# Performance work log

Hardware: AMD Instinct MI355X
Metric: run time of the kernel (lower is better)

Reference implementation:

```python
import jax, jax.numpy as jnp
import numpy as np

N = 100_000      # num nodes
E = 100_000      # num hyperedges
NNZ = 1_600_000  # incidence entries (avg degree 16)
DIN = 128
DOUT = 128


def setup_inputs() -> dict:
    key = jax.random.key(0)
    k1, k2, k3, k4 = jax.random.split(key, 4)
    x = jax.random.normal(k1, (N, DIN), dtype=jnp.float32)
    weight = jax.random.normal(k2, (DIN, DOUT), dtype=jnp.float32) / np.sqrt(DIN).astype(np.float32)
    bias = jax.random.normal(k3, (DOUT,), dtype=jnp.float32) * 0.02
    hyperedge_index = jax.random.randint(k4, (2, NNZ), 0, N, dtype=jnp.int64)
    return {"x": x, "weight": weight, "bias": bias, "hyperedge_index": hyperedge_index}


def reference(x, weight, bias, hyperedge_index):
    # PyG HypergraphConv (use_attention=False, heads=1):
    #   out = D^{-1} H W B^{-1} H^T (x @ Theta) + bias, W = I (unit hyperedge weights)
    node_idx = hyperedge_index[0]  # [NNZ]
    edge_idx = hyperedge_index[1]  # [NNZ]

    h = x @ weight  # [N, DOUT]

    ones = jnp.ones((NNZ,), dtype=h.dtype)
    # node degree D_i = sum of hyperedge weights (=1) over incident hyperedges
    D = jax.ops.segment_sum(ones, node_idx, num_segments=N)   # [N]
    # hyperedge degree B_e = number of incident nodes
    B = jax.ops.segment_sum(ones, edge_idx, num_segments=E)   # [E]
    Dinv = jnp.where(D > 0, 1.0 / D, 0.0)
    Binv = jnp.where(B > 0, 1.0 / B, 0.0)

    # nodes -> hyperedges: m_e = B_e^{-1} * sum_{i in e} h_i
    e_feat = jax.ops.segment_sum(h[node_idx], edge_idx, num_segments=E) * Binv[:, None]  # [E, DOUT]
    # hyperedges -> nodes: out_i = D_i^{-1} * sum_{e ni i} m_e
    out = jax.ops.segment_sum(e_feat[edge_idx], node_idx, num_segments=N) * Dinv[:, None]  # [N, DOUT]
    return out + bias
```

## Files before the change

kernel.cpp:

```cpp
#include <hip/hip_runtime.h>

#define Nn 100000
#define Ne 100000
#define NNZC 1600000
#define NBLK 256
#define CHUNK 6250
#define BSH 8
#define BUCKW 256
#define NBK 391
#define CAPB 5120
#define GEMM_TOTAL 1563
#define GEMM_A 782
#define GEMM_B 781
#define FCAP 4608
#define SEGW 4
#define NG0 6250

typedef __attribute__((ext_vector_type(8))) short short8;
typedef __attribute__((ext_vector_type(4))) float floatx4;

__device__ inline unsigned short f2bf(float f) {
    union { float f; unsigned int i; } c; c.f = f;
    unsigned int i = c.i;
    return (unsigned short)((i + 0x7fffu + ((i >> 16) & 1u)) >> 16);
}
__device__ inline unsigned int f2bf2(float lo, float hi) {
    union { float f; unsigned int i; } a, b;
    a.f = lo; b.f = hi;
    const unsigned int x = (a.i + 0x7fffu + ((a.i >> 16) & 1u)) >> 16;
    const unsigned int y = (b.i + 0x7fffu + ((b.i >> 16) & 1u)) & 0xffff0000u;
    return x | y;
}

union FusedLds {
    unsigned short wlds[128 * 136];
    struct { int a[NBK]; int b[NBK]; } s;
};
struct FineLds {
    int cnt[BUCKW];
    int tmp[2][BUCKW];
    unsigned int cache[FCAP];
};
union FineGemmLds {
    unsigned short wlds[128 * 136];
    FineLds f;
};

__device__ inline void gemm_block(int gb, const float* __restrict__ x,
                                  const float* __restrict__ w,
                                  unsigned short* __restrict__ h,
                                  unsigned short* wlds, int tid) {
    const int wave = tid >> 6, lane = tid & 63;
    const int q = lane >> 4, r16 = lane & 15;

    for (int i = tid; i < 4096; i += 256) {
        const int k = i >> 5;
        const int n0 = (i & 31) << 2;
        const float4 wv = *(const float4*)(w + k * 128 + n0);
        wlds[(n0 + 0) * 136 + k] = f2bf(wv.x);
        wlds[(n0 + 1) * 136 + k] = f2bf(wv.y);
        wlds[(n0 + 2) * 136 + k] = f2bf(wv.z);
        wlds[(n0 + 3) * 136 + k] = f2bf(wv.w);
    }
    __syncthreads();

    const int row0 = gb * 64 + wave * 16;
    const int rrow = min(row0 + r16, Nn - 1);

    floatx4 acc[8];
#pragma unroll
    for (int jb = 0; jb < 8; ++jb) acc[jb] = (floatx4){0.f, 0.f, 0.f, 0.f};

    const float* ap = x + (size_t)rrow * 128 + q * 8;
#pragma unroll
    for (int kk = 0; kk < 4; ++kk) {
        const float4 a0 = *(const float4*)(ap + kk * 32);
        const float4 a1 = *(const float4*)(ap + kk * 32 + 4);
        union { unsigned int u[4]; short8 s; } xf;
        xf.u[0] = f2bf2(a0.x, a0.y);
        xf.u[1] = f2bf2(a0.z, a0.w);
        xf.u[2] = f2bf2(a1.x, a1.y);
        xf.u[3] = f2bf2(a1.z, a1.w);
        const unsigned short* wp = wlds + kk * 32 + q * 8;
#pragma unroll
        for (int jb = 0; jb < 8; ++jb) {
            const short8 wf = *(const short8*)(wp + (jb * 16 + r16) * 136);
            acc[jb] = __builtin_amdgcn_mfma_f32_16x16x32_bf16(wf, xf.s, acc[jb], 0, 0, 0);
        }
    }

    if (row0 + r16 < Nn) {
        unsigned short* hb = h + (size_t)(row0 + r16) * 128 + q * 4;
#pragma unroll
        for (int jb = 0; jb < 8; ++jb) {
            uint2 o;
            o.x = f2bf2(acc[jb][0], acc[jb][1]);
            o.y = f2bf2(acc[jb][2], acc[jb][3]);
            *(uint2*)(hb + jb * 16) = o;
        }
    }
}

__global__ __launch_bounds__(256) void scatter_gemm_kernel(
        const int* __restrict__ nidx, const int* __restrict__ eidx,
        int* __restrict__ gcurN, int* __restrict__ gcurE,
        unsigned int* __restrict__ pairsN, unsigned int* __restrict__ pairsE,
        const float* __restrict__ x, const float* __restrict__ w,
        unsigned short* __restrict__ h) {
    __shared__ FusedLds sm;
    const int tid = threadIdx.x;
    if (blockIdx.x < NBLK) {
        for (int j = tid; j < NBK; j += 256) { sm.s.a[j] = 0; sm.s.b[j] = 0; }
        __syncthreads();
        const int base = blockIdx.x * CHUNK;
        for (int i = base + tid; i < base + CHUNK; i += 256) {
            atomicAdd(&sm.s.a[nidx[i] >> BSH], 1);
            atomicAdd(&sm.s.b[eidx[i] >> BSH], 1);
        }
        __syncthreads();
        for (int j = tid; j < NBK; j += 256) {
            sm.s.a[j] = atomicAdd(&gcurN[j], sm.s.a[j]);
            sm.s.b[j] = atomicAdd(&gcurE[j], sm.s.b[j]);
        }
        __syncthreads();
        for (int i = base + tid; i < base + CHUNK; i += 256) {
            const int n = nidx[i], e = eidx[i];
            const int pn = atomicAdd(&sm.s.a[n >> BSH], 1);
            if (pn < CAPB)
                pairsN[(size_t)(n >> BSH) * CAPB + pn] =
                    ((unsigned int)e << 8) | (unsigned int)(n & 255);
            const int pe = atomicAdd(&sm.s.b[e >> BSH], 1);
            if (pe < CAPB)
                pairsE[(size_t)(e >> BSH) * CAPB + pe] =
                    ((unsigned int)n << 8) | (unsigned int)(e & 255);
        }
    } else {
        gemm_block(blockIdx.x - NBLK, x, w, h, sm.wlds, tid);
    }
}

__device__ inline void fine_block(int b, const unsigned int* __restrict__ pairs,
                                  const int* __restrict__ gcur,
                                  int* __restrict__ offs, int* __restrict__ perm,
                                  FineLds& L, int t) {
    const int cnt_b = min(gcur[b], CAPB);
    int part = 0;
    for (int j = t; j < b; j += 256) part += min(gcur[j], CAPB);
    L.tmp[0][t] = part;
    __syncthreads();
    for (int off = 128; off > 0; off >>= 1) {
        if (t < off) L.tmp[0][t] += L.tmp[0][t + off];
        __syncthreads();
    }
    const int S = L.tmp[0][0];
    __syncthreads();

    const unsigned int* pb = pairs + (size_t)b * CAPB;
    L.cnt[t] = 0;
    __syncthreads();
    for (int i = t; i < cnt_b; i += BUCKW) {
        const unsigned int p = pb[i];
        if (i < FCAP) L.cache[i] = p;
        atomicAdd(&L.cnt[p & 255u], 1);
    }
    __syncthreads();
    int v = L.cnt[t];
    int pin = 0;
    L.tmp[0][t] = v;
    for (int off = 1; off < BUCKW; off <<= 1) {
        __syncthreads();
        int val = L.tmp[pin][t];
        if (t >= off) val += L.tmp[pin][t - off];
        L.tmp[1 - pin][t] = val;
        pin ^= 1;
    }
    __syncthreads();
    const int excl = L.tmp[pin][t] - v;
    const int id = b * BUCKW + t;
    if (id < 100000) offs[id] = S + excl;
    if (b == NBK - 1 && t == 0) offs[100000] = NNZC;
    __syncthreads();
    L.cnt[t] = excl;
    __syncthreads();
    for (int i = t; i < cnt_b; i += BUCKW) {
        const unsigned int p = (i < FCAP) ? L.cache[i] : pb[i];
        const int pos = S + atomicAdd(&L.cnt[p & 255u], 1);
        perm[pos] = (int)(p >> 8);
    }
}

template <int MODE>
__device__ inline void gather_body(int gblk, const int* __restrict__ perm,
                                   const int* __restrict__ offs,
                                   const void* __restrict__ srcv,
                                   const float* __restrict__ bias,
                                   void* __restrict__ outv, int tid) {
    const int wave = tid >> 6;
    const int lane = tid & 63;
    const int e0 = __builtin_amdgcn_readfirstlane((gblk * 4 + wave) * SEGW);
    const int start = offs[e0];
    const int end = offs[e0 + SEGW];
    const unsigned int laneoff = (unsigned int)lane << 2;
    const char* src = (const char*)srcv;

    float bx = 0.f, by = 0.f;
    if (MODE == 1) {
        const float2 b = ((const float2*)bias)[lane];
        bx = b.x; by = b.y;
    }

    float ax = 0.f, ay = 0.f;
    int e = e0;
    int seg_start = start;
    int nb = offs[e0 + 1];

    auto flush = [&](int deg) {
        const float sinv = deg ? 1.f / (float)deg : 0.f;
        if (MODE == 0) {
            *(unsigned int*)((char*)outv + (((unsigned int)e << 8) | laneoff)) =
                f2bf2(ax * sinv, ay * sinv);
        } else {
            float2 o;
            o.x = ax * sinv + bx;
            o.y = ay * sinv + by;
            *(float2*)((char*)outv + (((unsigned int)e << 9) | (laneoff << 1))) = o;
        }
        ax = 0.f; ay = 0.f;
        ++e;
    };

    int myv = 0;
    for (int i = start; i < end; i += 8) {
        const int t = (i - start) & 63;
        if (t == 0) myv = perm[min(i + lane, NNZC - 1)];
        const int m = min(end - i, 8);
        unsigned int a[8], u[8];
#pragma unroll
        for (int j = 0; j < 8; ++j)
            a[j] = ((unsigned int)__shfl(myv, t + (j < m ? j : m - 1), 64) << 8) | laneoff;
#pragma unroll
        for (int j = 0; j < 8; ++j) u[j] = *(const unsigned int*)(src + a[j]);
#pragma unroll
        for (int j = 0; j < 8; ++j) {
            if (j < m) {
                while (i + j == nb) {
                    flush(nb - seg_start);
                    seg_start = nb;
                    nb = offs[e + 1];
                }
                ax += __uint_as_float(u[j] << 16);
                ay += __uint_as_float(u[j] & 0xffff0000u);
            }
        }
    }
    while (e < e0 + SEGW) {
        flush(end - seg_start);
        seg_start = end;
    }
}

__global__ __launch_bounds__(256) void fineE_gemm_kernel(
        const unsigned int* __restrict__ pairsE, const int* __restrict__ gcurE,
        int* __restrict__ offsE, int* __restrict__ permE,
        const float* __restrict__ x, const float* __restrict__ w,
        unsigned short* __restrict__ h) {
    __shared__ FineGemmLds sm;
    const int tid = threadIdx.x;
    if (blockIdx.x < NBK) {
        fine_block(blockIdx.x, pairsE, gcurE, offsE, permE, sm.f, tid);
    } else {
        gemm_block(GEMM_A + blockIdx.x - NBK, x, w, h, sm.wlds, tid);
    }
}

__global__ __launch_bounds__(256) void g0_fineN_kernel(
        const int* __restrict__ permE, const int* __restrict__ offsE,
        const unsigned short* __restrict__ h, unsigned short* __restrict__ ef,
        const unsigned int* __restrict__ pairsN, const int* __restrict__ gcurN,
        int* __restrict__ offsN, int* __restrict__ permN) {
    __shared__ FineLds sm;
    const int tid = threadIdx.x;
    if (blockIdx.x < NBK) {
        fine_block(blockIdx.x, pairsN, gcurN, offsN, permN, sm, tid);
    } else {
        gather_body<0>(blockIdx.x - NBK, permE, offsE, h, nullptr, ef, tid);
    }
}

__global__ __launch_bounds__(256) void gather_e2n_kernel(
        const int* __restrict__ permN, const int* __restrict__ offsN,
        const unsigned short* __restrict__ ef, const float* __restrict__ bias,
        float* __restrict__ out) {
    gather_body<1>(blockIdx.x, permN, offsN, ef, bias, out, threadIdx.x);
}

extern "C" void kernel_launch(void* const* d_in, const int* in_sizes, int n_in,
                              void* d_out, int out_size, void* d_ws, size_t ws_size,
                              hipStream_t stream) {
    const float* x = (const float*)d_in[0];
    const float* w = (const float*)d_in[1];
    const float* bias = (const float*)d_in[2];
    const int* hei = (const int*)d_in[3];
    const int* nidx = hei;
    const int* eidx = hei + NNZC;
    float* out = (float*)d_out;

    char* p = (char*)d_ws;
    unsigned short* h = (unsigned short*)p;  p += (size_t)Nn * 128 * 2;
    unsigned short* ef = (unsigned short*)p; p += (size_t)Ne * 128 * 2;
    int* gcurN = (int*)p;                    p += NBK * 4 + 192;
    int* gcurE = (int*)p;                    p += NBK * 4 + 192;
    int* offsN = (int*)p;                    p += 400128;
    int* offsE = (int*)p;                    p += 400128;
    int* permN = (int*)p;                    p += (size_t)NNZC * 4;
    int* permE = (int*)p;                    p += (size_t)NNZC * 4;
    unsigned int* pairsN = (unsigned int*)p; p += (size_t)NBK * CAPB * 4;
    unsigned int* pairsE = (unsigned int*)p; p += (size_t)NBK * CAPB * 4;

    hipMemsetAsync(gcurN, 0, 2 * (NBK * 4 + 192), stream);

    scatter_gemm_kernel<<<NBLK + GEMM_A, 256, 0, stream>>>(nidx, eidx, gcurN, gcurE,
                                                           pairsN, pairsE, x, w, h);
    fineE_gemm_kernel<<<NBK + GEMM_B, 256, 0, stream>>>(pairsE, gcurE, offsE, permE,
                                                        x, w, h);
    g0_fineN_kernel<<<NBK + NG0, 256, 0, stream>>>(permE, offsE, h, ef,
                                                   pairsN, gcurN, offsN, permN);
    gather_e2n_kernel<<<NG0, 256, 0, stream>>>(permN, offsN, ef, bias, out);
}
```

Before: 297.7 us.

## Move GEMM out of scatter kernel and use 256-row GEMM blocks

Takes the GEMM blocks out of the scatter kernel, which now launches only the 256 scatter blocks. The whole GEMM moves into the second kernel alongside the E-side fine-sort blocks. Each GEMM block now covers 256 rows in four 64-row passes, so the weight-to-LDS bf16 conversion runs 391 times instead of 1563. This cuts redundant weight staging and changes which work overlaps, but the scatter kernel may leave the GPU underused and the GEMM now sits in a single kernel.

```diff
diff --git a/kernel.cpp b/kernel.cpp
--- a/kernel.cpp
+++ b/kernel.cpp
@@ -9,9 +9,7 @@
 #define BUCKW 256
 #define NBK 391
 #define CAPB 5120
-#define GEMM_TOTAL 1563
-#define GEMM_A 782
-#define GEMM_B 781
+#define GEMM_TOTAL 391
 #define FCAP 4608
 #define SEGW 4
 #define NG0 6250
@@ -32,10 +30,6 @@
     return x | y;
 }
 
-union FusedLds {
-    unsigned short wlds[128 * 136];
-    struct { int a[NBK]; int b[NBK]; } s;
-};
 struct FineLds {
     int cnt[BUCKW];
     int tmp[2][BUCKW];
@@ -46,10 +40,10 @@
     FineLds f;
 };
 
-__device__ inline void gemm_block(int gb, const float* __restrict__ x,
-                                  const float* __restrict__ w,
-                                  unsigned short* __restrict__ h,
-                                  unsigned short* wlds, int tid) {
+__device__ inline void gemm_block256(int gb, const float* __restrict__ x,
+                                     const float* __restrict__ w,
+                                     unsigned short* __restrict__ h,
+                                     unsigned short* wlds, int tid) {
     const int wave = tid >> 6, lane = tid & 63;
     const int q = lane >> 4, r16 = lane & 15;
 
@@ -64,78 +58,75 @@
     }
     __syncthreads();
 
-    const int row0 = gb * 64 + wave * 16;
-    const int rrow = min(row0 + r16, Nn - 1);
-
-    floatx4 acc[8];
-#pragma unroll
-    for (int jb = 0; jb < 8; ++jb) acc[jb] = (floatx4){0.f, 0.f, 0.f, 0.f};
-
-    const float* ap = x + (size_t)rrow * 128 + q * 8;
-#pragma unroll
-    for (int kk = 0; kk < 4; ++kk) {
-        const float4 a0 = *(const float4*)(ap + kk * 32);
-        const float4 a1 = *(const float4*)(ap + kk * 32 + 4);
-        union { unsigned int u[4]; short8 s; } xf;
-        xf.u[0] = f2bf2(a0.x, a0.y);
-        xf.u[1] = f2bf2(a0.z, a0.w);
-        xf.u[2] = f2bf2(a1.x, a1.y);
-        xf.u[3] = f2bf2(a1.z, a1.w);
-        const unsigned short* wp = wlds + kk * 32 + q * 8;
-#pragma unroll
-        for (int jb = 0; jb < 8; ++jb) {
-            const short8 wf = *(const short8*)(wp + (jb * 16 + r16) * 136);
-            acc[jb] = __builtin_amdgcn_mfma_f32_16x16x32_bf16(wf, xf.s, acc[jb], 0, 0, 0);
+#pragma unroll 1
+    for (int rg = 0; rg < 4; ++rg) {
+        const int row0 = gb * 256 + rg * 64 + wave * 16;
+        const int rrow = min(row0 + r16, Nn - 1);
+
+        floatx4 acc[8];
+#pragma unroll
+        for (int jb = 0; jb < 8; ++jb) acc[jb] = (floatx4){0.f, 0.f, 0.f, 0.f};
+
+        const float* ap = x + (size_t)rrow * 128 + q * 8;
+#pragma unroll
+        for (int kk = 0; kk < 4; ++kk) {
+            const float4 a0 = *(const float4*)(ap + kk * 32);
+            const float4 a1 = *(const float4*)(ap + kk * 32 + 4);
+            union { unsigned int u[4]; short8 s; } xf;
+            xf.u[0] = f2bf2(a0.x, a0.y);
+            xf.u[1] = f2bf2(a0.z, a0.w);
+            xf.u[2] = f2bf2(a1.x, a1.y);
+            xf.u[3] = f2bf2(a1.z, a1.w);
+            const unsigned short* wp = wlds + kk * 32 + q * 8;
+#pragma unroll
+            for (int jb = 0; jb < 8; ++jb) {
+                const short8 wf = *(const short8*)(wp + (jb * 16 + r16) * 136);
+                acc[jb] = __builtin_amdgcn_mfma_f32_16x16x32_bf16(wf, xf.s, acc[jb], 0, 0, 0);
+            }
         }
-    }
-
-    if (row0 + r16 < Nn) {
-        unsigned short* hb = h + (size_t)(row0 + r16) * 128 + q * 4;
-#pragma unroll
-        for (int jb = 0; jb < 8; ++jb) {
-            uint2 o;
-            o.x = f2bf2(acc[jb][0], acc[jb][1]);
-            o.y = f2bf2(acc[jb][2], acc[jb][3]);
-            *(uint2*)(hb + jb * 16) = o;
+
+        if (row0 + r16 < Nn) {
+            unsigned short* hb = h + (size_t)(row0 + r16) * 128 + q * 4;
+#pragma unroll
+            for (int jb = 0; jb < 8; ++jb) {
+                uint2 o;
+                o.x = f2bf2(acc[jb][0], acc[jb][1]);
+                o.y = f2bf2(acc[jb][2], acc[jb][3]);
+                *(uint2*)(hb + jb * 16) = o;
+            }
         }
     }
 }
 
-__global__ __launch_bounds__(256) void scatter_gemm_kernel(
+__global__ __launch_bounds__(256) void scatter_kernel(
         const int* __restrict__ nidx, const int* __restrict__ eidx,
         int* __restrict__ gcurN, int* __restrict__ gcurE,
-        unsigned int* __restrict__ pairsN, unsigned int* __restrict__ pairsE,
-        const float* __restrict__ x, const float* __restrict__ w,
-        unsigned short* __restrict__ h) {
-    __shared__ FusedLds sm;
+        unsigned int* __restrict__ pairsN, unsigned int* __restrict__ pairsE) {
+    __shared__ struct { int a[NBK]; int b[NBK]; } sm;
     const int tid = threadIdx.x;
-    if (blockIdx.x < NBLK) {
-        for (int j = tid; j < NBK; j += 256) { sm.s.a[j] = 0; sm.s.b[j] = 0; }
-        __syncthreads();
-        const int base = blockIdx.x * CHUNK;
-        for (int i = base + tid; i < base + CHUNK; i += 256) {
-            atomicAdd(&sm.s.a[nidx[i] >> BSH], 1);
-            atomicAdd(&sm.s.b[eidx[i] >> BSH], 1);
-        }
-        __syncthreads();
-        for (int j = tid; j < NBK; j += 256) {
-            sm.s.a[j] = atomicAdd(&gcurN[j], sm.s.a[j]);
-            sm.s.b[j] = atomicAdd(&gcurE[j], sm.s.b[j]);
-        }
-        __syncthreads();
-        for (int i = base + tid; i < base + CHUNK; i += 256) {
-            const int n = nidx[i], e = eidx[i];
-            const int pn = atomicAdd(&sm.s.a[n >> BSH], 1);
-            if (pn < CAPB)
-                pairsN[(size_t)(n >> BSH) * CAPB + pn] =
-                    ((unsigned int)e << 8) | (unsigned int)(n & 255);
-            const int pe = atomicAdd(&sm.s.b[e >> BSH], 1);
-            if (pe < CAPB)
-                pairsE[(size_t)(e >> BSH) * CAPB + pe] =
-                    ((unsigned int)n << 8) | (unsigned int)(e & 255);
-        }
-    } else {
-        gemm_block(blockIdx.x - NBLK, x, w, h, sm.wlds, tid);
+    for (int j = tid; j < NBK; j += 256) { sm.a[j] = 0; sm.b[j] = 0; }
+    __syncthreads();
+    const int base = blockIdx.x * CHUNK;
+    for (int i = base + tid; i < base + CHUNK; i += 256) {
+        atomicAdd(&sm.a[nidx[i] >> BSH], 1);
+        atomicAdd(&sm.b[eidx[i] >> BSH], 1);
+    }
+    __syncthreads();
+    for (int j = tid; j < NBK; j += 256) {
+        sm.a[j] = atomicAdd(&gcurN[j], sm.a[j]);
+        sm.b[j] = atomicAdd(&gcurE[j], sm.b[j]);
+    }
+    __syncthreads();
+    for (int i = base + tid; i < base + CHUNK; i += 256) {
+        const int n = nidx[i], e = eidx[i];
+        const int pn = atomicAdd(&sm.a[n >> BSH], 1);
+        if (pn < CAPB)
+            pairsN[(size_t)(n >> BSH) * CAPB + pn] =
+                ((unsigned int)e << 8) | (unsigned int)(n & 255);
+        const int pe = atomicAdd(&sm.b[e >> BSH], 1);
+        if (pe < CAPB)
+            pairsE[(size_t)(e >> BSH) * CAPB + pe] =
+                ((unsigned int)n << 8) | (unsigned int)(e & 255);
     }
 }
 
@@ -259,17 +250,17 @@
     }
 }
 
-__global__ __launch_bounds__(256) void fineE_gemm_kernel(
+__global__ __launch_bounds__(256) void gemmE_kernel(
+        const float* __restrict__ x, const float* __restrict__ w,
+        unsigned short* __restrict__ h,
         const unsigned int* __restrict__ pairsE, const int* __restrict__ gcurE,
-        int* __restrict__ offsE, int* __restrict__ permE,
-        const float* __restrict__ x, const float* __restrict__ w,
-        unsigned short* __restrict__ h) {
+        int* __restrict__ offsE, int* __restrict__ permE) {
     __shared__ FineGemmLds sm;
     const int tid = threadIdx.x;
-    if (blockIdx.x < NBK) {
-        fine_block(blockIdx.x, pairsE, gcurE, offsE, permE, sm.f, tid);
+    if (blockIdx.x < GEMM_TOTAL) {
+        gemm_block256(blockIdx.x, x, w, h, sm.wlds, tid);
     } else {
-        gemm_block(GEMM_A + blockIdx.x - NBK, x, w, h, sm.wlds, tid);
+        fine_block(blockIdx.x - GEMM_TOTAL, pairsE, gcurE, offsE, permE, sm.f, tid);
     }
 }
 
@@ -319,10 +310,9 @@
 
     hipMemsetAsync(gcurN, 0, 2 * (NBK * 4 + 192), stream);
 
-    scatter_gemm_kernel<<<NBLK + GEMM_A, 256, 0, stream>>>(nidx, eidx, gcurN, gcurE,
-                                                           pairsN, pairsE, x, w, h);
-    fineE_gemm_kernel<<<NBK + GEMM_B, 256, 0, stream>>>(pairsE, gcurE, offsE, permE,
-                                                        x, w, h);
+    scatter_kernel<<<NBLK, 256, 0, stream>>>(nidx, eidx, gcurN, gcurE, pairsN, pairsE);
+    gemmE_kernel<<<GEMM_TOTAL + NBK, 256, 0, stream>>>(x, w, h, pairsE, gcurE,
+                                                       offsE, permE);
     g0_fineN_kernel<<<NBK + NG0, 256, 0, stream>>>(permE, offsE, h, ef,
                                                    pairsN, gcurN, offsN, permN);
     gather_e2n_kernel<<<NG0, 256, 0, stream>>>(permN, offsN, ef, bias, out);
```

Result: no change. 297.1 us (-0.2%).
